# Performance work log

Hardware: AMD Instinct MI355X
Metric: run time of the kernel (lower is better)

The kernel has to match this reference:

```python
import jax, jax.numpy as jnp
import numpy as np

B, T, C, H = 2, 2048, 1024, 16
HD = C // H  # head dim = 64


def setup_inputs() -> dict:
    key = jax.random.key(0)
    k0, k1, k2 = jax.random.split(key, 3)
    x = jax.random.normal(k0, (B, T, C), jnp.float32)
    W_attn = jax.random.normal(k1, (C, 3 * C), jnp.float32) * 0.02
    b_attn = jnp.zeros((3 * C,), jnp.float32)
    W_proj = jax.random.normal(k2, (C, C), jnp.float32) * 0.02
    b_proj = jnp.zeros((C,), jnp.float32)
    # causal mask, broadcast over (B, H) like torch masked_fill(~mask)
    attn_mask = jnp.tril(jnp.ones((T, T), dtype=bool))[None, None]
    return {"x": x, "W_attn": W_attn, "b_attn": b_attn,
            "W_proj": W_proj, "b_proj": b_proj, "attn_mask": attn_mask}


def _rotate_half(x):
    # interleaved rotate_half as in rotary-embedding-torch: (x1,x2)->(-x2,x1)
    x1 = x[..., 0::2]
    x2 = x[..., 1::2]
    return jnp.stack((-x2, x1), axis=-1).reshape(x.shape)


def _apply_rope(x):
    # x: [B, H, T, HD]
    hd = x.shape[-1]
    t = x.shape[-2]
    inv_freq = 1.0 / (10000.0 ** (jnp.arange(0, hd, 2, dtype=jnp.float32) / hd))
    freqs = jnp.arange(t, dtype=jnp.float32)[:, None] * inv_freq[None, :]  # [T, HD/2]
    freqs = jnp.repeat(freqs, 2, axis=-1)  # [T, HD], interleaved
    return x * jnp.cos(freqs) + _rotate_half(x) * jnp.sin(freqs)


def reference(x, W_attn, b_attn, W_proj, b_proj, attn_mask):
    Bb, Tt, Cc = x.shape
    qkv = x @ W_attn + b_attn                     # [B, T, 3C]
    q, k, v = jnp.split(qkv, 3, axis=-1)

    def to_heads(z):
        return z.reshape(Bb, Tt, H, HD).transpose(0, 2, 1, 3)  # [B, H, T, HD]

    q, k, v = to_heads(q), to_heads(k), to_heads(v)
    q = _apply_rope(q)
    k = _apply_rope(k)

    scale = 1.0 / jnp.sqrt(jnp.float32(HD))
    att = jnp.einsum('bhqd,bhkd->bhqk', q, k) * scale  # [B, H, T, T]
    att = jnp.where(attn_mask, att, jnp.float32(-10000.0))
    att = jax.nn.softmax(att, axis=-1)
    # dropout = 0.0 (eval): identity
    y = jnp.einsum('bhqk,bhkd->bhqd', att, v)           # [B, H, T, HD]
    y = y.transpose(0, 2, 1, 3).reshape(Bb, Tt, Cc)
    return y @ W_proj + b_proj
```

## Files before the change

### kernel.cpp

```cpp
#include <hip/hip_runtime.h>

#define B_ 2
#define T_ 2048
#define C_ 1024
#define H_ 16
#define HD_ 64

typedef unsigned short u16;
typedef unsigned int u32;
typedef __attribute__((ext_vector_type(8))) short short8;
typedef __attribute__((ext_vector_type(4))) float f32x4;
typedef __attribute__((ext_vector_type(2))) u32 uint2v;
typedef __attribute__((ext_vector_type(4))) u32 uint4v;

typedef __attribute__((address_space(1))) const void* as1cv;
typedef __attribute__((address_space(3))) void* as3v;

__device__ __forceinline__ u16 f2bf(float x){
  union { float f; u32 u; } v; v.f = x;
  u32 r = v.u + 0x7fffu + ((v.u >> 16) & 1u);
  return (u16)(r >> 16);
}
__device__ __forceinline__ float bf2f(u16 h){
  union { u32 u; float f; } v; v.u = ((u32)h) << 16;
  return v.f;
}
__device__ __forceinline__ u32 cvt_pk_bf16(float lo, float hi){
  u32 r;
  asm("v_cvt_pk_bf16_f32 %0, %1, %2" : "=v"(r) : "v"(lo), "v"(hi));
  return r;
}
__device__ __forceinline__ void gl_lds16(const u16* src, u16* dst){
  __builtin_amdgcn_global_load_lds((as1cv)src, (as3v)dst, 16, 0, 0);
}

__global__ void k_conv(const float* __restrict__ in, u16* __restrict__ out){
  int i = blockIdx.x * 256 + threadIdx.x;
  f32x4 v = ((const f32x4*)in)[i];
  uint2v o;
  o.x = (u32)f2bf(v.x) | ((u32)f2bf(v.y) << 16);
  o.y = (u32)f2bf(v.z) | ((u32)f2bf(v.w) << 16);
  ((uint2v*)out)[i] = o;
}

__global__ void k_transpose(const float* __restrict__ in, u16* __restrict__ out,
                            int R, int Cc){
  __shared__ float tile[32][33];
  int c0 = blockIdx.x * 32, r0 = blockIdx.y * 32;
  int tx = threadIdx.x, ty = threadIdx.y;
#pragma unroll
  for (int ii = 0; ii < 4; ++ii)
    tile[ty + ii*8][tx] = in[(size_t)(r0 + ty + ii*8) * Cc + c0 + tx];
  __syncthreads();
#pragma unroll
  for (int ii = 0; ii < 4; ++ii)
    out[(size_t)(c0 + ty + ii*8) * R + r0 + tx] = f2bf(tile[tx][ty + ii*8]);
}

__global__ __launch_bounds__(256, 2)
void k_gemm0(const u16* __restrict__ A, const u16* __restrict__ Bt,
             const float* __restrict__ bias, u16* __restrict__ outb,
             u16* __restrict__ vt, int M, int N, int K)
{
  __shared__ u16 As[128*64];
  __shared__ u16 Bs[128*64];
  int nwg = gridDim.x;
  int cpx = nwg >> 3;
  int bid = blockIdx.x;
  int wg = (bid & 7) * cpx + (bid >> 3);
  int ntn = N >> 7;
  int m0 = (wg / ntn) << 7, n0 = (wg % ntn) << 7;
  int tid = threadIdx.x;
  int lane = tid & 63, w = tid >> 6;
  int c = lane & 15, g = lane >> 4;
  int wr = w >> 1, wc = w & 1;

  f32x4 z4 = {0.f,0.f,0.f,0.f};
  f32x4 acc[4][4];
#pragma unroll
  for (int i=0;i<4;++i)
#pragma unroll
    for (int j=0;j<4;++j) acc[i][j] = z4;

  u16* dstA = As + ((tid & 0xC0) << 3);
  u16* dstB = Bs + ((tid & 0xC0) << 3);

  for (int k0 = 0; k0 < K; k0 += 64){
#pragma unroll
    for (int it = 0; it < 4; ++it){
      int ch = it*256 + tid;
      int row = ch >> 3, slot = ch & 7;
      gl_lds16(A + (size_t)(m0+row)*K + k0 + slot*8, dstA + it*2048);
    }
#pragma unroll
    for (int it = 0; it < 4; ++it){
      int ch = it*256 + tid;
      int row = ch >> 3, slot = ch & 7;
      gl_lds16(Bt + (size_t)(n0+row)*K + k0 + slot*8, dstB + it*2048);
    }
    __syncthreads();
#pragma unroll
    for (int ks = 0; ks < 2; ++ks){
      short8 af[4], bf[4];
#pragma unroll
      for (int i=0;i<4;++i)
        af[i] = *(const short8*)(As + (wr*64 + i*16 + c)*64 + ks*32 + g*8);
#pragma unroll
      for (int j=0;j<4;++j)
        bf[j] = *(const short8*)(Bs + (wc*64 + j*16 + c)*64 + ks*32 + g*8);
#pragma unroll
      for (int i=0;i<4;++i)
#pragma unroll
        for (int j=0;j<4;++j)
          acc[i][j] = __builtin_amdgcn_mfma_f32_16x16x32_bf16(af[i], bf[j], acc[i][j], 0, 0, 0);
    }
    __syncthreads();
  }

  if (n0 >= 2048){
#pragma unroll
    for (int i=0;i<4;++i){
      int rowb = m0 + wr*64 + i*16 + g*4;
      int bb = rowb >> 11, t0 = rowb & 2047;
#pragma unroll
      for (int j=0;j<4;++j){
        int col = n0 + wc*64 + j*16 + c;
        float bv = bias[col];
        int vc = col - 2048;
        int hh = vc >> 6, d = vc & 63;
        uint2v o;
        o.x = (u32)f2bf(acc[i][j].x + bv) | ((u32)f2bf(acc[i][j].y + bv) << 16);
        o.y = (u32)f2bf(acc[i][j].z + bv) | ((u32)f2bf(acc[i][j].w + bv) << 16);
        *(uint2v*)(vt + ((size_t)((bb*16 + hh)*64 + d))*2048 + t0) = o;
      }
    }
  } else {
#pragma unroll
    for (int i=0;i<4;++i){
#pragma unroll
      for (int j=0;j<4;++j){
        int col = n0 + wc*64 + j*16 + c;
        float bv = bias[col];
#pragma unroll
        for (int r=0;r<4;++r){
          int row = m0 + wr*64 + i*16 + g*4 + r;
          outb[(size_t)row*2048 + col] = f2bf(acc[i][j][r] + bv);
        }
      }
    }
  }
}

__global__ __launch_bounds__(256, 2)
void k_gemmp(const u16* __restrict__ A, const u16* __restrict__ Bt,
             const float* __restrict__ bias, float* __restrict__ outf)
{
  __shared__ u16 As[128*64];
  __shared__ u16 Bs[64*64];
  const int K = 1024, N = 1024;
  int nwg = gridDim.x;
  int cpx = nwg >> 3;
  int bid = blockIdx.x;
  int wg = (bid & 7) * cpx + (bid >> 3);
  int m0 = (wg >> 4) << 7, n0 = (wg & 15) << 6;
  int tid = threadIdx.x;
  int lane = tid & 63, w = tid >> 6;
  int c = lane & 15, g = lane >> 4;
  int wr = w >> 1, wc = w & 1;

  f32x4 z4 = {0.f,0.f,0.f,0.f};
  f32x4 acc[4][2];
#pragma unroll
  for (int i=0;i<4;++i)
#pragma unroll
    for (int j=0;j<2;++j) acc[i][j] = z4;

  u16* dstA = As + ((tid & 0xC0) << 3);
  u16* dstB = Bs + ((tid & 0xC0) << 3);

  for (int k0 = 0; k0 < K; k0 += 64){
#pragma unroll
    for (int it = 0; it < 4; ++it){
      int ch = it*256 + tid;
      int row = ch >> 3, slot = ch & 7;
      gl_lds16(A + (size_t)(m0+row)*K + k0 + slot*8, dstA + it*2048);
    }
#pragma unroll
    for (int it = 0; it < 2; ++it){
      int ch = it*256 + tid;
      int row = ch >> 3, slot = ch & 7;
      gl_lds16(Bt + (size_t)(n0+row)*K + k0 + slot*8, dstB + it*2048);
    }
    __syncthreads();
#pragma unroll
    for (int ks = 0; ks < 2; ++ks){
      short8 af[4], bf[2];
#pragma unroll
      for (int i=0;i<4;++i)
        af[i] = *(const short8*)(As + (wr*64 + i*16 + c)*64 + ks*32 + g*8);
#pragma unroll
      for (int j=0;j<2;++j)
        bf[j] = *(const short8*)(Bs + (wc*32 + j*16 + c)*64 + ks*32 + g*8);
#pragma unroll
      for (int i=0;i<4;++i)
#pragma unroll
        for (int j=0;j<2;++j)
          acc[i][j] = __builtin_amdgcn_mfma_f32_16x16x32_bf16(af[i], bf[j], acc[i][j], 0, 0, 0);
    }
    __syncthreads();
  }

#pragma unroll
  for (int i=0;i<4;++i){
#pragma unroll
    for (int j=0;j<2;++j){
      int col = n0 + wc*32 + j*16 + c;
      float bv = bias[col];
#pragma unroll
      for (int r=0;r<4;++r){
        int row = m0 + wr*64 + i*16 + g*4 + r;
        outf[(size_t)row*N + col] = acc[i][j][r] + bv;
      }
    }
  }
}

__global__ void k_rope(const u16* __restrict__ qkv, u16* __restrict__ Qh,
                       u16* __restrict__ Kh){
  int idx = blockIdx.x * 256 + threadIdx.x;
  int sec = idx >> 21;
  int p = idx & 0x1FFFFF;
  int row = p >> 9;
  int ii = p & 511;
  int h = ii >> 5, ip = ii & 31;
  int t = row & 2047;
  int b = row >> 11;
  float invf = exp2f((float)(-2 * ip) * (1.f/64.f) * 13.287712379549449f);
  float th = (float)t * invf;
  float sn, cs;
  sincosf(th, &sn, &cs);
  u32 v = *(const u32*)(qkv + (size_t)row*2048 + sec*1024 + h*64 + 2*ip);
  float x0 = bf2f((u16)(v & 0xFFFFu));
  float x1 = bf2f((u16)(v >> 16));
  float y0 = x0*cs - x1*sn;
  float y1 = x1*cs + x0*sn;
  if (sec == 0){ y0 *= 0.180336880f; y1 *= 0.180336880f; }
  u32 o = (u32)f2bf(y0) | ((u32)f2bf(y1) << 16);
  u16* dst = sec ? Kh : Qh;
  *(u32*)(dst + ((size_t)((b*16 + h)*2048 + t))*64 + 2*ip) = o;
}

__global__ __launch_bounds__(256, 3)
void k_attn(const u16* __restrict__ Qh, const u16* __restrict__ Kh,
            const u16* __restrict__ Vt, u16* __restrict__ Pb,
            float* __restrict__ lp)
{
  __shared__ u16 KV[4*4096];
  __shared__ u16 Ps[4*32*64];

  int bid = blockIdx.x;
  int qt = 15 - (bid >> 7);
  int r7 = bid & 127;
  int ck = r7 >> 5, bh = r7 & 31;
  int q0 = qt << 7;
  int tid = threadIdx.x, lane = tid & 63, w = tid >> 6;
  int c = lane & 15, g = lane >> 4;
  int q0w = q0 + w*32;
  int nt = (qt + 1) << 1;
  int t0 = (nt * ck) >> 2;
  int t1 = (nt * (ck + 1)) >> 2;

  const u16* Kbase = Kh + (size_t)bh * T_ * 64;
  const u16* Vbase = Vt + (size_t)bh * 64 * T_;
  const u16* Qbase = Qh + (size_t)bh * T_ * 64;

  short8 qf[2][2];
#pragma unroll
  for (int qs=0;qs<2;++qs)
#pragma unroll
    for (int ks=0;ks<2;++ks)
      qf[qs][ks] = *(const short8*)(Qbase + (size_t)(q0w + qs*16 + c)*64 + ks*32 + g*8);

  f32x4 z4 = {0.f,0.f,0.f,0.f};
  f32x4 acc[2][4];
#pragma unroll
  for (int qs=0;qs<2;++qs)
#pragma unroll
    for (int ds=0;ds<4;++ds) acc[qs][ds] = z4;
  float psum[2] = {0.f, 0.f};

  char* PsB = (char*)Ps + w*4096;

  int row2[2], soff2[2];
  u16* dst0[2];
#pragma unroll
  for (int it=0; it<2; ++it){
    int ch = it*256 + tid;
    row2[it] = ch >> 3;
    int slot = ch & 7;
    soff2[it] = (slot ^ (row2[it] & 7)) << 3;
    dst0[it] = KV + ((it*256 + (tid & 0xC0)) << 3);
  }

  if (t0 < t1){
    int kv0 = t0 << 6;
#pragma unroll
    for (int it=0; it<2; ++it){
      gl_lds16(Kbase + (size_t)(kv0 + row2[it])*64 + soff2[it], dst0[it]);
      gl_lds16(Vbase + (size_t)row2[it]*T_ + kv0 + soff2[it], dst0[it] + 2*4096);
    }
  }
  __syncthreads();

  for (int t = t0; t < t1; ++t){
    int cur = (t - t0) & 1;
    int kv0 = t << 6;
    if (t + 1 < t1){
      int kvn = kv0 + 64;
      int nxt = cur ^ 1;
#pragma unroll
      for (int it=0; it<2; ++it){
        gl_lds16(Kbase + (size_t)(kvn + row2[it])*64 + soff2[it], dst0[it] + nxt*4096);
        gl_lds16(Vbase + (size_t)row2[it]*T_ + kvn + soff2[it], dst0[it] + (2+nxt)*4096);
      }
    }

    if (kv0 <= q0w + 31){
      const char* KsC = (const char*)(KV + cur*4096);
      const char* VsC = (const char*)(KV + (2+cur)*4096);

      f32x4 st[4][2];
#pragma unroll
      for (int kv=0;kv<4;++kv)
#pragma unroll
        for (int qs=0;qs<2;++qs) st[kv][qs] = z4;

#pragma unroll
      for (int ks=0;ks<2;++ks){
        short8 kf[4];
#pragma unroll
        for (int kv=0;kv<4;++kv){
          int row = kv*16 + c;
          kf[kv] = *(const short8*)(KsC + row*128 + (((ks*4+g) ^ (row&7)) << 4));
        }
#pragma unroll
        for (int kv=0;kv<4;++kv)
#pragma unroll
          for (int qs=0;qs<2;++qs)
            st[kv][qs] = __builtin_amdgcn_mfma_f32_16x16x32_bf16(kf[kv], qf[qs][ks], st[kv][qs], 0, 0, 0);
      }

      if (kv0 + 63 > q0w){
#pragma unroll
        for (int kv=0;kv<4;++kv)
#pragma unroll
          for (int qs=0;qs<2;++qs)
#pragma unroll
            for (int r=0;r<4;++r){
              int kvi = kv0 + kv*16 + g*4 + r;
              int qi = q0w + qs*16 + c;
              if (kvi > qi) st[kv][qs][r] = -INFINITY;
            }
      }

#pragma unroll
      for (int qs=0;qs<2;++qs){
        float s01 = 0.f, s23 = 0.f;
#pragma unroll
        for (int kv=0;kv<4;++kv){
          float e0 = __builtin_amdgcn_exp2f(st[kv][qs][0]);
          float e1 = __builtin_amdgcn_exp2f(st[kv][qs][1]);
          float e2 = __builtin_amdgcn_exp2f(st[kv][qs][2]);
          float e3 = __builtin_amdgcn_exp2f(st[kv][qs][3]);
          st[kv][qs][0] = e0; st[kv][qs][1] = e1;
          st[kv][qs][2] = e2; st[kv][qs][3] = e3;
          s01 += e0 + e1; s23 += e2 + e3;
        }
        psum[qs] += s01 + s23;
        int q = qs*16 + c;
#pragma unroll
        for (int kv=0;kv<4;++kv){
          uint2v o;
          o.x = cvt_pk_bf16(st[kv][qs][0], st[kv][qs][1]);
          o.y = cvt_pk_bf16(st[kv][qs][2], st[kv][qs][3]);
          *(uint2v*)(PsB + q*128 + ((kv*32 + g*8) ^ ((q&7) << 4))) = o;
        }
      }

#pragma unroll
      for (int ks=0;ks<2;++ks){
        short8 vb[4];
#pragma unroll
        for (int ds=0;ds<4;++ds){
          int row = ds*16 + c;
          vb[ds] = *(const short8*)(VsC + row*128 + (((ks*4+g) ^ (row&7)) << 4));
        }
#pragma unroll
        for (int qs=0;qs<2;++qs){
          int q = qs*16 + c;
          short8 pa = *(const short8*)(PsB + q*128 + (((ks*4+g) << 4) ^ ((q&7) << 4)));
#pragma unroll
          for (int ds=0;ds<4;++ds)
            acc[qs][ds] = __builtin_amdgcn_mfma_f32_16x16x32_bf16(pa, vb[ds], acc[qs][ds], 0, 0, 0);
        }
      }
    }

    __syncthreads();
  }

#pragma unroll
  for (int qs=0;qs<2;++qs){
    psum[qs] += __shfl_xor(psum[qs], 16);
    psum[qs] += __shfl_xor(psum[qs], 32);
  }
  if (g == 0){
    lp[ck*65536 + bh*2048 + q0w + c]      = psum[0];
    lp[ck*65536 + bh*2048 + q0w + 16 + c] = psum[1];
  }
#pragma unroll
  for (int qs=0;qs<2;++qs){
#pragma unroll
    for (int r=0;r<4;++r){
      int trow = q0w + qs*16 + g*4 + r;
      size_t off = (((size_t)(ck*32 + bh)*2048) + trow)*64;
#pragma unroll
      for (int ds=0;ds<4;++ds)
        Pb[off + ds*16 + c] = f2bf(acc[qs][ds][r]);
    }
  }
}

__global__ void k_merge(const u16* __restrict__ Pb, const float* __restrict__ lp,
                        u16* __restrict__ Y)
{
  int idx = blockIdx.x * 256 + threadIdx.x;
  int d8 = idx & 7;
  int t  = (idx >> 3) & 2047;
  int bh = idx >> 14;
  int lt = bh*2048 + t;
  float l = lp[lt] + lp[lt + 65536] + lp[lt + 131072] + lp[lt + 196608];
  float inv = 1.0f / l;
  float s[8] = {0.f,0.f,0.f,0.f,0.f,0.f,0.f,0.f};
#pragma unroll
  for (int ck=0; ck<4; ++ck){
    short8 p = *(const short8*)(Pb + (((size_t)(ck*32 + bh)*2048 + t) << 6) + d8*8);
#pragma unroll
    for (int j=0;j<8;++j) s[j] += bf2f((u16)p[j]);
  }
  uint4v o;
  o.x = cvt_pk_bf16(s[0]*inv, s[1]*inv);
  o.y = cvt_pk_bf16(s[2]*inv, s[3]*inv);
  o.z = cvt_pk_bf16(s[4]*inv, s[5]*inv);
  o.w = cvt_pk_bf16(s[6]*inv, s[7]*inv);
  int bb = bh >> 4, hh = bh & 15;
  *(uint4v*)(Y + ((size_t)(bb*2048 + t))*1024 + hh*64 + d8*8) = o;
}

extern "C" void kernel_launch(void* const* d_in, const int* in_sizes, int n_in,
                              void* d_out, int out_size, void* d_ws, size_t ws_size,
                              hipStream_t stream)
{
  const float* x  = (const float*)d_in[0];
  const float* Wa = (const float*)d_in[1];
  const float* ba = (const float*)d_in[2];
  const float* Wp = (const float*)d_in[3];
  const float* bp = (const float*)d_in[4];
  float* out = (float*)d_out;
  char* ws = (char*)d_ws;

  u16* xb  = (u16*)(ws);
  u16* WaT = (u16*)(ws + (8u  << 20));
  u16* qkv = (u16*)(ws + (16u << 20));
  u16* Pb  = (u16*)(ws);
  u16* Qh  = (u16*)(ws + (32u << 20));
  u16* Y   = Qh;
  u16* Kh  = (u16*)(ws + (40u << 20));
  u16* Vt  = (u16*)(ws + (48u << 20));
  u16* WpT = (u16*)(ws + (56u << 20));
  float* lp = (float*)(ws + (58u << 20));

  k_conv<<<4096, 256, 0, stream>>>(x, xb);
  k_transpose<<<dim3(96,32), dim3(32,8), 0, stream>>>(Wa, WaT, 1024, 3072);
  k_transpose<<<dim3(32,32), dim3(32,8), 0, stream>>>(Wp, WpT, 1024, 1024);
  k_gemm0<<<768, 256, 0, stream>>>(xb, WaT, ba, qkv, Vt, 4096, 3072, 1024);
  k_rope<<<16384, 256, 0, stream>>>(qkv, Qh, Kh);
  k_attn<<<2048, 256, 0, stream>>>(Qh, Kh, Vt, Pb, lp);
  k_merge<<<2048, 256, 0, stream>>>(Pb, lp, Y);
  k_gemmp<<<512, 256, 0, stream>>>(Y, WpT, bp, out);
}
```

Before: 119.2 us.

## Rewrite QKV GEMM with 256x128 tiles, triple-buffered swizzled LDS pipeline

Reworks the QKV projection GEMM to use 512-thread workgroups computing 256x128 tiles. Global-to-LDS loads are triple-buffered two K-steps ahead, with vmcnt waits and barriers interleaved between MFMA phases. LDS rows are XOR-swizzled to avoid bank conflicts, and s_setprio raises priority around the MFMA block. This aims to hide load latency and remove the full syncthreads stalls, at the cost of 144KB LDS per block (one block per CU) and a grid halved to 384 blocks.

```diff
diff --git a/kernel.cpp b/kernel.cpp
--- a/kernel.cpp
+++ b/kernel.cpp
@@ -57,24 +57,43 @@
     out[(size_t)(c0 + ty + ii*8) * R + r0 + tx] = f2bf(tile[tx][ty + ii*8]);
 }
 
-__global__ __launch_bounds__(256, 2)
-void k_gemm0(const u16* __restrict__ A, const u16* __restrict__ Bt,
+__global__ __launch_bounds__(512, 1)
+void k_gemm0(const u16* __restrict__ Ag, const u16* __restrict__ Bg,
              const float* __restrict__ bias, u16* __restrict__ outb,
              u16* __restrict__ vt, int M, int N, int K)
 {
-  __shared__ u16 As[128*64];
-  __shared__ u16 Bs[128*64];
+  __shared__ u16 LDSM[73728];
+  const int nk = K >> 6;
   int nwg = gridDim.x;
   int cpx = nwg >> 3;
   int bid = blockIdx.x;
   int wg = (bid & 7) * cpx + (bid >> 3);
   int ntn = N >> 7;
-  int m0 = (wg / ntn) << 7, n0 = (wg % ntn) << 7;
+  int m0 = (wg / ntn) << 8, n0 = (wg % ntn) << 7;
   int tid = threadIdx.x;
   int lane = tid & 63, w = tid >> 6;
   int c = lane & 15, g = lane >> 4;
   int wr = w >> 1, wc = w & 1;
 
+  int rowA[4], soffA[4], ldsA[4];
+#pragma unroll
+  for (int ia=0; ia<4; ++ia){
+    int ch = ia*512 + tid;
+    rowA[ia] = ch >> 3;
+    soffA[ia] = ((ch & 7) ^ (rowA[ia] & 7)) << 3;
+    ldsA[ia] = ia*4096 + (tid & 0x1C0)*8;
+  }
+  int rowB[2], soffB[2], ldsB[2];
+#pragma unroll
+  for (int ib=0; ib<2; ++ib){
+    int ch = ib*512 + tid;
+    rowB[ib] = ch >> 3;
+    soffB[ib] = ((ch & 7) ^ (rowB[ib] & 7)) << 3;
+    ldsB[ib] = 49152 + ib*4096 + (tid & 0x1C0)*8;
+  }
+  const u16* Abase = Ag + (size_t)m0*K;
+  const u16* Bbase = Bg + (size_t)n0*K;
+
   f32x4 z4 = {0.f,0.f,0.f,0.f};
   f32x4 acc[4][4];
 #pragma unroll
@@ -82,69 +101,101 @@
 #pragma unroll
     for (int j=0;j<4;++j) acc[i][j] = z4;
 
-  u16* dstA = As + ((tid & 0xC0) << 3);
-  u16* dstB = Bs + ((tid & 0xC0) << 3);
-
-  for (int k0 = 0; k0 < K; k0 += 64){
-#pragma unroll
-    for (int it = 0; it < 4; ++it){
-      int ch = it*256 + tid;
-      int row = ch >> 3, slot = ch & 7;
-      gl_lds16(A + (size_t)(m0+row)*K + k0 + slot*8, dstA + it*2048);
-    }
-#pragma unroll
-    for (int it = 0; it < 4; ++it){
-      int ch = it*256 + tid;
-      int row = ch >> 3, slot = ch & 7;
-      gl_lds16(Bt + (size_t)(n0+row)*K + k0 + slot*8, dstB + it*2048);
-    }
-    __syncthreads();
-#pragma unroll
-    for (int ks = 0; ks < 2; ++ks){
+  int c7 = c & 7;
+  int aoff0 = (wr*64 + c)*64;
+  int boff0 = (wc*64 + c)*64;
+
+#pragma unroll
+  for (int ia=0; ia<4; ++ia)
+    gl_lds16(Abase + (size_t)rowA[ia]*K + soffA[ia], (u16*)LDSM + ldsA[ia]);
+#pragma unroll
+  for (int ib=0; ib<2; ++ib)
+    gl_lds16(Bbase + (size_t)rowB[ib]*K + soffB[ib], (u16*)LDSM + ldsB[ib]);
+#pragma unroll
+  for (int ia=0; ia<4; ++ia)
+    gl_lds16(Abase + (size_t)rowA[ia]*K + 64 + soffA[ia], (u16*)LDSM + 16384 + ldsA[ia]);
+#pragma unroll
+  for (int ib=0; ib<2; ++ib)
+    gl_lds16(Bbase + (size_t)rowB[ib]*K + 64 + soffB[ib], (u16*)LDSM + 8192 + ldsB[ib]);
+  asm volatile("s_waitcnt vmcnt(6)" ::: "memory");
+  __builtin_amdgcn_s_barrier();
+  __builtin_amdgcn_sched_barrier(0);
+
+  for (int kt = 0; kt < nk; ++kt){
+    int buf = kt % 3;
+    const u16* Ab = (const u16*)LDSM + buf*16384;
+    const u16* Bb = (const u16*)LDSM + 49152 + buf*8192;
+    int sbuf = (kt + 2) % 3;
+    bool dostage = (kt + 2 < nk);
+#pragma unroll
+    for (int ks=0; ks<2; ++ks){
       short8 af[4], bf[4];
-#pragma unroll
-      for (int i=0;i<4;++i)
-        af[i] = *(const short8*)(As + (wr*64 + i*16 + c)*64 + ks*32 + g*8);
-#pragma unroll
-      for (int j=0;j<4;++j)
-        bf[j] = *(const short8*)(Bs + (wc*64 + j*16 + c)*64 + ks*32 + g*8);
-#pragma unroll
-      for (int i=0;i<4;++i)
-#pragma unroll
-        for (int j=0;j<4;++j)
-          acc[i][j] = __builtin_amdgcn_mfma_f32_16x16x32_bf16(af[i], bf[j], acc[i][j], 0, 0, 0);
-    }
-    __syncthreads();
+      int sx = ((ks*4 + g) ^ c7) << 3;
+#pragma unroll
+      for (int mf=0; mf<4; ++mf)
+        af[mf] = *(const short8*)(Ab + aoff0 + mf*1024 + sx);
+#pragma unroll
+      for (int nf=0; nf<4; ++nf)
+        bf[nf] = *(const short8*)(Bb + boff0 + nf*1024 + sx);
+      if (dostage){
+        if (ks == 0){
+#pragma unroll
+          for (int ia=0; ia<4; ++ia)
+            gl_lds16(Abase + (size_t)rowA[ia]*K + (kt+2)*64 + soffA[ia],
+                     (u16*)LDSM + sbuf*16384 + ldsA[ia]);
+        } else {
+#pragma unroll
+          for (int ib=0; ib<2; ++ib)
+            gl_lds16(Bbase + (size_t)rowB[ib]*K + (kt+2)*64 + soffB[ib],
+                     (u16*)LDSM + sbuf*8192 + ldsB[ib]);
+        }
+      }
+      __builtin_amdgcn_s_barrier();
+      __builtin_amdgcn_sched_barrier(0);
+      __builtin_amdgcn_s_setprio(1);
+#pragma unroll
+      for (int mf=0; mf<4; ++mf)
+#pragma unroll
+        for (int nf=0; nf<4; ++nf)
+          acc[mf][nf] = __builtin_amdgcn_mfma_f32_16x16x32_bf16(af[mf], bf[nf], acc[mf][nf], 0, 0, 0);
+      __builtin_amdgcn_s_setprio(0);
+      if (ks == 1 && kt < nk-1){
+        if (dostage) asm volatile("s_waitcnt vmcnt(6)" ::: "memory");
+        else         asm volatile("s_waitcnt vmcnt(0)" ::: "memory");
+      }
+      __builtin_amdgcn_s_barrier();
+      __builtin_amdgcn_sched_barrier(0);
+    }
   }
 
   if (n0 >= 2048){
 #pragma unroll
-    for (int i=0;i<4;++i){
-      int rowb = m0 + wr*64 + i*16 + g*4;
+    for (int mf=0; mf<4; ++mf){
+      int rowb = m0 + wr*64 + mf*16 + g*4;
       int bb = rowb >> 11, t0 = rowb & 2047;
 #pragma unroll
-      for (int j=0;j<4;++j){
-        int col = n0 + wc*64 + j*16 + c;
+      for (int nf=0; nf<4; ++nf){
+        int col = n0 + wc*64 + nf*16 + c;
         float bv = bias[col];
         int vc = col - 2048;
         int hh = vc >> 6, d = vc & 63;
         uint2v o;
-        o.x = (u32)f2bf(acc[i][j].x + bv) | ((u32)f2bf(acc[i][j].y + bv) << 16);
-        o.y = (u32)f2bf(acc[i][j].z + bv) | ((u32)f2bf(acc[i][j].w + bv) << 16);
+        o.x = (u32)f2bf(acc[mf][nf].x + bv) | ((u32)f2bf(acc[mf][nf].y + bv) << 16);
+        o.y = (u32)f2bf(acc[mf][nf].z + bv) | ((u32)f2bf(acc[mf][nf].w + bv) << 16);
         *(uint2v*)(vt + ((size_t)((bb*16 + hh)*64 + d))*2048 + t0) = o;
       }
     }
   } else {
 #pragma unroll
-    for (int i=0;i<4;++i){
-#pragma unroll
-      for (int j=0;j<4;++j){
-        int col = n0 + wc*64 + j*16 + c;
+    for (int mf=0; mf<4; ++mf){
+#pragma unroll
+      for (int nf=0; nf<4; ++nf){
+        int col = n0 + wc*64 + nf*16 + c;
         float bv = bias[col];
 #pragma unroll
-        for (int r=0;r<4;++r){
-          int row = m0 + wr*64 + i*16 + g*4 + r;
-          outb[(size_t)row*2048 + col] = f2bf(acc[i][j][r] + bv);
+        for (int r=0; r<4; ++r){
+          int row = m0 + wr*64 + mf*16 + g*4 + r;
+          outb[(size_t)row*2048 + col] = f2bf(acc[mf][nf][r] + bv);
         }
       }
     }
@@ -483,7 +534,7 @@
   k_conv<<<4096, 256, 0, stream>>>(x, xb);
   k_transpose<<<dim3(96,32), dim3(32,8), 0, stream>>>(Wa, WaT, 1024, 3072);
   k_transpose<<<dim3(32,32), dim3(32,8), 0, stream>>>(Wp, WpT, 1024, 1024);
-  k_gemm0<<<768, 256, 0, stream>>>(xb, WaT, ba, qkv, Vt, 4096, 3072, 1024);
+  k_gemm0<<<384, 512, 0, stream>>>(xb, WaT, ba, qkv, Vt, 4096, 3072, 1024);
   k_rope<<<16384, 256, 0, stream>>>(qkv, Qh, Kh);
   k_attn<<<2048, 256, 0, stream>>>(Qh, Kh, Vt, Pb, lp);
   k_merge<<<2048, 256, 0, stream>>>(Pb, lp, Y);
```

After: 124.1 us. 1.04x slower.
